# Kernel tuning notes

Hardware: AMD Instinct MI355X
Metric: run time of the kernel (lower is better)

Reference implementation:

```python
import jax, jax.numpy as jnp
import numpy as np

EPS = 1e-12  # F.normalize default eps (norm clamped to at least eps)


def setup_inputs() -> dict:
    key = jax.random.key(0)
    k1, k2, k3, k4 = jax.random.split(key, 4)
    B, Cin, Cout, H, W = 8, 128, 32, 256, 256
    x = jax.random.normal(k1, (B, Cin, H, W), dtype=jnp.float32)
    qk = jax.random.normal(k2, (B, 2 * Cout, H, W), dtype=jnp.float32)
    # 1x1 conv params (PyTorch Conv2d default init scale ~ 1/sqrt(fan_in))
    w_v = jax.random.normal(k3, (Cout, Cin), dtype=jnp.float32) / np.sqrt(Cin)
    b_v = jax.random.normal(k4, (Cout,), dtype=jnp.float32) / np.sqrt(Cin)
    temperature = jnp.ones((1, 1, 1), dtype=jnp.float32)
    return {"x": x, "qk": qk, "w_v": w_v, "b_v": b_v, "temperature": temperature}


def reference(x, qk, w_v, b_v, temperature):
    B, Cin, H, W = x.shape
    Co = w_v.shape[0]
    N = H * W
    # 1x1 conv == channel GEMM
    v = jnp.einsum('bchw,oc->bohw', x, w_v) + b_v[None, :, None, None]
    # split qk: k = first Co channels, q = last Co channels; head=1
    q = qk[:, Co:].reshape(B, 1, Co, N)
    k = qk[:, :Co].reshape(B, 1, Co, N)
    v = v.reshape(B, 1, Co, N)
    # L2-normalize over spatial dim (F.normalize: divide by max(norm, eps))
    q = q / jnp.maximum(jnp.linalg.norm(q, axis=-1, keepdims=True), EPS)
    k = k / jnp.maximum(jnp.linalg.norm(k, axis=-1, keepdims=True), EPS)
    # channel-wise (transposed) attention: [B,1,Co,Co]
    attn = jnp.einsum('bhcn,bhdn->bhcd', q, k) * temperature
    attn = jax.nn.softmax(attn, axis=-1)
    out = jnp.einsum('bhcd,bhdn->bhcn', attn, v)  # [B,1,Co,N]
    return out
```

## Files before the change

### kernel.cpp

```cpp
#include <hip/hip_runtime.h>
#include <math.h>

#define NB    8
#define CIN   128
#define CO    32
#define CH    64
#define NN    65536
#define CHUNKS 128
#define COLS_PB (NN/CHUNKS)
#define TILE  32
#define LSTR  72

__global__ __launch_bounds__(256) void gram_kernel(const float* __restrict__ qk,
                                                   float* __restrict__ part,
                                                   float* __restrict__ partsq) {
    __shared__ float lds[TILE * LSTR];
    __shared__ float red[4 * 1024 + 4 * 64];

    const int t = threadIdx.x;
    const int b = blockIdx.y;
    const int chunk = blockIdx.x;

    const int c = t >> 2;
    const int g = t & 3;

    const int w = t >> 6;
    const int lane = t & 63;
    const int l16 = lane & 15;
    const int colsub = lane >> 4;
    const int qi0 = 32 + (l16 >> 2) * 8;
    const int ki0 = (l16 & 3) * 8;

    const float* src = qk + (size_t)b * CH * NN + (size_t)chunk * COLS_PB + (size_t)c * NN;

    float acc[8][8];
#pragma unroll
    for (int i = 0; i < 8; ++i)
#pragma unroll
        for (int j = 0; j < 8; ++j) acc[i][j] = 0.f;
    float sqa[4] = {0.f, 0.f, 0.f, 0.f};

    for (int tile = 0; tile < COLS_PB / TILE; ++tile) {
        const float4* s4 = (const float4*)(src + tile * TILE);
        float4 v0 = s4[g * 2];
        float4 v1 = s4[g * 2 + 1];

        __syncthreads();
        float* dst = &lds[(g * 8) * LSTR + c];
        dst[0 * LSTR] = v0.x; dst[1 * LSTR] = v0.y; dst[2 * LSTR] = v0.z; dst[3 * LSTR] = v0.w;
        dst[4 * LSTR] = v1.x; dst[5 * LSTR] = v1.y; dst[6 * LSTR] = v1.z; dst[7 * LSTR] = v1.w;
        __syncthreads();

#pragma unroll
        for (int p = 0; p < 2; ++p) {
            const float* row = &lds[(w * 8 + p * 4 + colsub) * LSTR];
            float4 q0 = *(const float4*)(row + qi0);
            float4 q1 = *(const float4*)(row + qi0 + 4);
            float4 k0 = *(const float4*)(row + ki0);
            float4 k1 = *(const float4*)(row + ki0 + 4);
            float qv[8] = {q0.x, q0.y, q0.z, q0.w, q1.x, q1.y, q1.z, q1.w};
            float kv[8] = {k0.x, k0.y, k0.z, k0.w, k1.x, k1.y, k1.z, k1.w};
#pragma unroll
            for (int i = 0; i < 8; ++i)
#pragma unroll
                for (int j = 0; j < 8; ++j)
                    acc[i][j] = fmaf(qv[i], kv[j], acc[i][j]);
            float4 sv = *(const float4*)(row + l16 * 4);
            sqa[0] = fmaf(sv.x, sv.x, sqa[0]);
            sqa[1] = fmaf(sv.y, sv.y, sqa[1]);
            sqa[2] = fmaf(sv.z, sv.z, sqa[2]);
            sqa[3] = fmaf(sv.w, sv.w, sqa[3]);
        }
    }

#pragma unroll
    for (int i = 0; i < 8; ++i)
#pragma unroll
        for (int j = 0; j < 8; ++j) {
            acc[i][j] += __shfl_xor(acc[i][j], 16);
            acc[i][j] += __shfl_xor(acc[i][j], 32);
        }
#pragma unroll
    for (int s = 0; s < 4; ++s) {
        sqa[s] += __shfl_xor(sqa[s], 16);
        sqa[s] += __shfl_xor(sqa[s], 32);
    }

    if (colsub == 0) {
#pragma unroll
        for (int i = 0; i < 8; ++i)
#pragma unroll
            for (int j = 0; j < 8; ++j)
                red[w * 1024 + l16 * 64 + i * 8 + j] = acc[i][j];
#pragma unroll
        for (int s = 0; s < 4; ++s)
            red[4096 + w * 64 + l16 * 4 + s] = sqa[s];
    }
    __syncthreads();

    for (int idx = t; idx < 1024; idx += 256) {
        float s = red[idx] + red[1024 + idx] + red[2048 + idx] + red[3072 + idx];
        int lw = idx >> 6;
        int i = (idx >> 3) & 7;
        int j = idx & 7;
        int qrel = (lw >> 2) * 8 + i;
        int krel = (lw & 3) * 8 + j;
        part[((size_t)b * CHUNKS + chunk) * 1024 + qrel * 32 + krel] = s;
    }
    if (t < 64) {
        float s = red[4096 + t] + red[4096 + 64 + t] + red[4096 + 128 + t] + red[4096 + 192 + t];
        partsq[((size_t)b * CHUNKS + chunk) * 64 + t] = s;
    }
}

__global__ __launch_bounds__(128) void reduce_kernel(const float* __restrict__ part,
                                                     const float* __restrict__ partsq,
                                                     float* __restrict__ Sred) {
    const int b = blockIdx.y;
    const int v = blockIdx.x * 64 + (threadIdx.x >> 1);
    const int h = threadIdx.x & 1;
    float s = 0.f;
    if (v < 1024) {
        const float* p = part + (size_t)b * CHUNKS * 1024 + v;
        for (int ch = h * (CHUNKS / 2); ch < (h + 1) * (CHUNKS / 2); ++ch)
            s += p[(size_t)ch * 1024];
    } else {
        const float* p = partsq + (size_t)b * CHUNKS * 64 + (v - 1024);
        for (int ch = h * (CHUNKS / 2); ch < (h + 1) * (CHUNKS / 2); ++ch)
            s += p[(size_t)ch * 64];
    }
    s += __shfl_xor(s, 1);
    if (h == 0) Sred[b * 1088 + v] = s;
}

__global__ __launch_bounds__(256) void attn_kernel(const float* __restrict__ Sred,
                                                   const float* __restrict__ w_v,
                                                   const float* __restrict__ b_v,
                                                   const float* __restrict__ temp,
                                                   float* __restrict__ Weff,
                                                   float* __restrict__ beff) {
    __shared__ float sS[1024];
    __shared__ float snorm[64];
    __shared__ float sA[1024];
    const int t = threadIdx.x;
    const int b = blockIdx.x;

    for (int i = t; i < 1024; i += 256) sS[i] = Sred[b * 1088 + i];
    if (t < 64) snorm[t] = fmaxf(sqrtf(Sred[b * 1088 + 1024 + t]), 1e-12f);
    __syncthreads();

    if (t < 32) {
        const float T = temp[0];
        const float qn = snorm[32 + t];
        float m = -1e30f;
        for (int d = 0; d < 32; ++d)
            m = fmaxf(m, sS[t * 32 + d] / (qn * snorm[d]) * T);
        float sum = 0.f;
        for (int d = 0; d < 32; ++d)
            sum += expf(sS[t * 32 + d] / (qn * snorm[d]) * T - m);
        const float inv = 1.f / sum;
        for (int d = 0; d < 32; ++d)
            sA[t * 32 + d] = expf(sS[t * 32 + d] / (qn * snorm[d]) * T - m) * inv;
    }
    __syncthreads();

    for (int idx = t; idx < CO * CIN; idx += 256) {
        int cc = idx >> 7;
        int ci = idx & 127;
        float s = 0.f;
#pragma unroll
        for (int d = 0; d < 32; ++d) s += sA[cc * 32 + d] * w_v[d * CIN + ci];
        Weff[(size_t)b * CO * CIN + idx] = s;
    }
    if (t < 32) {
        float s = 0.f;
#pragma unroll
        for (int d = 0; d < 32; ++d) s += sA[t * 32 + d] * b_v[d];
        beff[b * CO + t] = s;
    }
}

__global__ __launch_bounds__(256) void out_kernel(const float* __restrict__ x,
                                                  const float* __restrict__ Weff,
                                                  const float* __restrict__ beff,
                                                  float* __restrict__ out) {
    const int b = blockIdx.y;
    const int n0 = blockIdx.x * 512 + threadIdx.x * 2;
    const float* xb = x + (size_t)b * CIN * NN + n0;
    const float* Wb = Weff + (size_t)b * CO * CIN;
    const float* bb = beff + b * CO;

    float a0[CO], a1[CO];
#pragma unroll
    for (int o = 0; o < CO; ++o) { a0[o] = bb[o]; a1[o] = bb[o]; }

#pragma unroll 4
    for (int ci = 0; ci < CIN; ++ci) {
        float2 xv = *(const float2*)(xb + (size_t)ci * NN);
#pragma unroll
        for (int o = 0; o < CO; ++o) {
            float wv = Wb[o * CIN + ci];
            a0[o] = fmaf(wv, xv.x, a0[o]);
            a1[o] = fmaf(wv, xv.y, a1[o]);
        }
    }

    float* ob = out + (size_t)b * CO * NN + n0;
#pragma unroll
    for (int o = 0; o < CO; ++o) {
        float2 r;
        r.x = a0[o];
        r.y = a1[o];
        *(float2*)(ob + (size_t)o * NN) = r;
    }
}

extern "C" void kernel_launch(void* const* d_in, const int* in_sizes, int n_in,
                              void* d_out, int out_size, void* d_ws, size_t ws_size,
                              hipStream_t stream) {
    const float* x    = (const float*)d_in[0];
    const float* qk   = (const float*)d_in[1];
    const float* w_v  = (const float*)d_in[2];
    const float* b_v  = (const float*)d_in[3];
    const float* temp = (const float*)d_in[4];
    float* out = (float*)d_out;

    float* part   = (float*)d_ws;
    float* partsq = part + (size_t)NB * CHUNKS * 1024;
    float* Sred   = partsq + (size_t)NB * CHUNKS * 64;
    float* Weff   = Sred + (size_t)NB * 1088;
    float* beff   = Weff + (size_t)NB * CO * CIN;

    gram_kernel<<<dim3(CHUNKS, NB), 256, 0, stream>>>(qk, part, partsq);
    reduce_kernel<<<dim3(17, NB), 128, 0, stream>>>(part, partsq, Sred);
    attn_kernel<<<dim3(NB), 256, 0, stream>>>(Sred, w_v, b_v, temp, Weff, beff);
    out_kernel<<<dim3(NN / 512, NB), 256, 0, stream>>>(x, Weff, beff, out);
}
```

Before: 133.2 us.

## Fuse partial reduction into attention kernel and retile output GEMM with LDS weights

```diff
diff --git a/kernel.cpp b/kernel.cpp
--- a/kernel.cpp
+++ b/kernel.cpp
@@ -113,40 +113,35 @@
     }
 }
 
-__global__ __launch_bounds__(128) void reduce_kernel(const float* __restrict__ part,
-                                                     const float* __restrict__ partsq,
-                                                     float* __restrict__ Sred) {
-    const int b = blockIdx.y;
-    const int v = blockIdx.x * 64 + (threadIdx.x >> 1);
-    const int h = threadIdx.x & 1;
-    float s = 0.f;
-    if (v < 1024) {
-        const float* p = part + (size_t)b * CHUNKS * 1024 + v;
-        for (int ch = h * (CHUNKS / 2); ch < (h + 1) * (CHUNKS / 2); ++ch)
-            s += p[(size_t)ch * 1024];
-    } else {
-        const float* p = partsq + (size_t)b * CHUNKS * 64 + (v - 1024);
-        for (int ch = h * (CHUNKS / 2); ch < (h + 1) * (CHUNKS / 2); ++ch)
-            s += p[(size_t)ch * 64];
-    }
-    s += __shfl_xor(s, 1);
-    if (h == 0) Sred[b * 1088 + v] = s;
-}
-
-__global__ __launch_bounds__(256) void attn_kernel(const float* __restrict__ Sred,
-                                                   const float* __restrict__ w_v,
-                                                   const float* __restrict__ b_v,
-                                                   const float* __restrict__ temp,
-                                                   float* __restrict__ Weff,
-                                                   float* __restrict__ beff) {
+__global__ __launch_bounds__(256) void finalize_kernel(const float* __restrict__ part,
+                                                       const float* __restrict__ partsq,
+                                                       const float* __restrict__ w_v,
+                                                       const float* __restrict__ b_v,
+                                                       const float* __restrict__ temp,
+                                                       float* __restrict__ Weff,
+                                                       float* __restrict__ beff) {
     __shared__ float sS[1024];
     __shared__ float snorm[64];
     __shared__ float sA[1024];
     const int t = threadIdx.x;
     const int b = blockIdx.x;
 
-    for (int i = t; i < 1024; i += 256) sS[i] = Sred[b * 1088 + i];
-    if (t < 64) snorm[t] = fmaxf(sqrtf(Sred[b * 1088 + 1024 + t]), 1e-12f);
+    for (int v = t; v < 1024; v += 256) {
+        const float* p = part + (size_t)b * CHUNKS * 1024 + v;
+        float s = 0.f;
+#pragma unroll 16
+        for (int ch = 0; ch < CHUNKS; ++ch)
+            s += p[(size_t)ch * 1024];
+        sS[v] = s;
+    }
+    if (t < 64) {
+        const float* p = partsq + (size_t)b * CHUNKS * 64 + t;
+        float s = 0.f;
+#pragma unroll 16
+        for (int ch = 0; ch < CHUNKS; ++ch)
+            s += p[(size_t)ch * 64];
+        snorm[t] = fmaxf(sqrtf(s), 1e-12f);
+    }
     __syncthreads();
 
     if (t < 32) {
@@ -184,35 +179,58 @@
                                                   const float* __restrict__ Weff,
                                                   const float* __restrict__ beff,
                                                   float* __restrict__ out) {
+    __shared__ float4 lw[CO * 32];
     const int b = blockIdx.y;
-    const int n0 = blockIdx.x * 512 + threadIdx.x * 2;
+    const int t = threadIdx.x;
+
+    {
+        const float4* Wb4 = (const float4*)(Weff + (size_t)b * CO * CIN);
+        for (int i = t; i < CO * 32; i += 256) lw[i] = Wb4[i];
+    }
+    __syncthreads();
+
+    const int n0 = blockIdx.x * 1024 + t * 4;
     const float* xb = x + (size_t)b * CIN * NN + n0;
-    const float* Wb = Weff + (size_t)b * CO * CIN;
     const float* bb = beff + b * CO;
 
-    float a0[CO], a1[CO];
-#pragma unroll
-    for (int o = 0; o < CO; ++o) { a0[o] = bb[o]; a1[o] = bb[o]; }
-
-#pragma unroll 4
-    for (int ci = 0; ci < CIN; ++ci) {
-        float2 xv = *(const float2*)(xb + (size_t)ci * NN);
+    float4 acc[CO];
+#pragma unroll
+    for (int o = 0; o < CO; ++o) {
+        float bv = bb[o];
+        acc[o] = make_float4(bv, bv, bv, bv);
+    }
+
+    for (int ci4 = 0; ci4 < 32; ++ci4) {
+        float4 xv0 = *(const float4*)(xb + (size_t)(ci4 * 4 + 0) * NN);
+        float4 xv1 = *(const float4*)(xb + (size_t)(ci4 * 4 + 1) * NN);
+        float4 xv2 = *(const float4*)(xb + (size_t)(ci4 * 4 + 2) * NN);
+        float4 xv3 = *(const float4*)(xb + (size_t)(ci4 * 4 + 3) * NN);
 #pragma unroll
         for (int o = 0; o < CO; ++o) {
-            float wv = Wb[o * CIN + ci];
-            a0[o] = fmaf(wv, xv.x, a0[o]);
-            a1[o] = fmaf(wv, xv.y, a1[o]);
+            float4 w = lw[o * 32 + ci4];
+            acc[o].x = fmaf(w.x, xv0.x, acc[o].x);
+            acc[o].y = fmaf(w.x, xv0.y, acc[o].y);
+            acc[o].z = fmaf(w.x, xv0.z, acc[o].z);
+            acc[o].w = fmaf(w.x, xv0.w, acc[o].w);
+            acc[o].x = fmaf(w.y, xv1.x, acc[o].x);
+            acc[o].y = fmaf(w.y, xv1.y, acc[o].y);
+            acc[o].z = fmaf(w.y, xv1.z, acc[o].z);
+            acc[o].w = fmaf(w.y, xv1.w, acc[o].w);
+            acc[o].x = fmaf(w.z, xv2.x, acc[o].x);
+            acc[o].y = fmaf(w.z, xv2.y, acc[o].y);
+            acc[o].z = fmaf(w.z, xv2.z, acc[o].z);
+            acc[o].w = fmaf(w.z, xv2.w, acc[o].w);
+            acc[o].x = fmaf(w.w, xv3.x, acc[o].x);
+            acc[o].y = fmaf(w.w, xv3.y, acc[o].y);
+            acc[o].z = fmaf(w.w, xv3.z, acc[o].z);
+            acc[o].w = fmaf(w.w, xv3.w, acc[o].w);
         }
     }
 
     float* ob = out + (size_t)b * CO * NN + n0;
 #pragma unroll
-    for (int o = 0; o < CO; ++o) {
-        float2 r;
-        r.x = a0[o];
-        r.y = a1[o];
-        *(float2*)(ob + (size_t)o * NN) = r;
-    }
+    for (int o = 0; o < CO; ++o)
+        *(float4*)(ob + (size_t)o * NN) = acc[o];
 }
 
 extern "C" void kernel_launch(void* const* d_in, const int* in_sizes, int n_in,
@@ -227,12 +245,10 @@
 
     float* part   = (float*)d_ws;
     float* partsq = part + (size_t)NB * CHUNKS * 1024;
-    float* Sred   = partsq + (size_t)NB * CHUNKS * 64;
-    float* Weff   = Sred + (size_t)NB * 1088;
+    float* Weff   = partsq + (size_t)NB * CHUNKS * 64;
     float* beff   = Weff + (size_t)NB * CO * CIN;
 
     gram_kernel<<<dim3(CHUNKS, NB), 256, 0, stream>>>(qk, part, partsq);
-    reduce_kernel<<<dim3(17, NB), 128, 0, stream>>>(part, partsq, Sred);
-    attn_kernel<<<dim3(NB), 256, 0, stream>>>(Sred, w_v, b_v, temp, Weff, beff);
-    out_kernel<<<dim3(NN / 512, NB), 256, 0, stream>>>(x, Weff, beff, out);
-}
+    finalize_kernel<<<dim3(NB), 256, 0, stream>>>(part, partsq, w_v, b_v, temp, Weff, beff);
+    out_kernel<<<dim3(NN / 1024, NB), 256, 0, stream>>>(x, Weff, beff, out);
+}
```

Result: slower. 161.2 us (+21.0%).

## Compute Gram matrix with split-bf16 MFMA per wave instead of LDS FMA tiles

Applied to the files above, without the earlier changes.

```diff
diff --git a/kernel.cpp b/kernel.cpp
--- a/kernel.cpp
+++ b/kernel.cpp
@@ -1,4 +1,5 @@
 #include <hip/hip_runtime.h>
+#include <hip/hip_bf16.h>
 #include <math.h>
 
 #define NB    8
@@ -7,109 +8,82 @@
 #define CH    64
 #define NN    65536
 #define CHUNKS 128
-#define COLS_PB (NN/CHUNKS)
-#define TILE  32
-#define LSTR  72
+#define GXB   32
+#define SPW   (NN/CHUNKS)
+#define SLABS (SPW/16)
+
+typedef __attribute__((ext_vector_type(8))) short bf16x8;
+typedef __attribute__((ext_vector_type(16))) float f32x16;
+
+__device__ __forceinline__ short f2bf(float f) {
+    union { __hip_bfloat16 h; short s; } u;
+    u.h = __float2bfloat16(f);
+    return u.s;
+}
+__device__ __forceinline__ float bf2f(short s) {
+    union { __hip_bfloat16 h; short s; } u;
+    u.s = s;
+    return __bfloat162float(u.h);
+}
 
 __global__ __launch_bounds__(256) void gram_kernel(const float* __restrict__ qk,
                                                    float* __restrict__ part,
                                                    float* __restrict__ partsq) {
-    __shared__ float lds[TILE * LSTR];
-    __shared__ float red[4 * 1024 + 4 * 64];
-
-    const int t = threadIdx.x;
     const int b = blockIdx.y;
-    const int chunk = blockIdx.x;
-
-    const int c = t >> 2;
-    const int g = t & 3;
-
-    const int w = t >> 6;
-    const int lane = t & 63;
-    const int l16 = lane & 15;
-    const int colsub = lane >> 4;
-    const int qi0 = 32 + (l16 >> 2) * 8;
-    const int ki0 = (l16 & 3) * 8;
-
-    const float* src = qk + (size_t)b * CH * NN + (size_t)chunk * COLS_PB + (size_t)c * NN;
-
-    float acc[8][8];
-#pragma unroll
-    for (int i = 0; i < 8; ++i)
-#pragma unroll
-        for (int j = 0; j < 8; ++j) acc[i][j] = 0.f;
-    float sqa[4] = {0.f, 0.f, 0.f, 0.f};
-
-    for (int tile = 0; tile < COLS_PB / TILE; ++tile) {
-        const float4* s4 = (const float4*)(src + tile * TILE);
-        float4 v0 = s4[g * 2];
-        float4 v1 = s4[g * 2 + 1];
-
-        __syncthreads();
-        float* dst = &lds[(g * 8) * LSTR + c];
-        dst[0 * LSTR] = v0.x; dst[1 * LSTR] = v0.y; dst[2 * LSTR] = v0.z; dst[3 * LSTR] = v0.w;
-        dst[4 * LSTR] = v1.x; dst[5 * LSTR] = v1.y; dst[6 * LSTR] = v1.z; dst[7 * LSTR] = v1.w;
-        __syncthreads();
-
-#pragma unroll
-        for (int p = 0; p < 2; ++p) {
-            const float* row = &lds[(w * 8 + p * 4 + colsub) * LSTR];
-            float4 q0 = *(const float4*)(row + qi0);
-            float4 q1 = *(const float4*)(row + qi0 + 4);
-            float4 k0 = *(const float4*)(row + ki0);
-            float4 k1 = *(const float4*)(row + ki0 + 4);
-            float qv[8] = {q0.x, q0.y, q0.z, q0.w, q1.x, q1.y, q1.z, q1.w};
-            float kv[8] = {k0.x, k0.y, k0.z, k0.w, k1.x, k1.y, k1.z, k1.w};
-#pragma unroll
-            for (int i = 0; i < 8; ++i)
-#pragma unroll
-                for (int j = 0; j < 8; ++j)
-                    acc[i][j] = fmaf(qv[i], kv[j], acc[i][j]);
-            float4 sv = *(const float4*)(row + l16 * 4);
-            sqa[0] = fmaf(sv.x, sv.x, sqa[0]);
-            sqa[1] = fmaf(sv.y, sv.y, sqa[1]);
-            sqa[2] = fmaf(sv.z, sv.z, sqa[2]);
-            sqa[3] = fmaf(sv.w, sv.w, sqa[3]);
+    const int w = threadIdx.x >> 6;
+    const int l = threadIdx.x & 63;
+    const int chunk = blockIdx.x * 4 + w;
+    const int c = l & 31;
+    const int half = l >> 5;
+
+    const float* qrow = qk + (size_t)b * CH * NN + (size_t)(CO + c) * NN
+                        + (size_t)chunk * SPW + half * 8;
+    const float* krow = qk + (size_t)b * CH * NN + (size_t)c * NN
+                        + (size_t)chunk * SPW + half * 8;
+
+    f32x16 acc = {};
+    float sqq = 0.f, sqk = 0.f;
+
+#pragma unroll 4
+    for (int s = 0; s < SLABS; ++s) {
+        float4 q0 = *(const float4*)(qrow + s * 16);
+        float4 q1 = *(const float4*)(qrow + s * 16 + 4);
+        float4 k0 = *(const float4*)(krow + s * 16);
+        float4 k1 = *(const float4*)(krow + s * 16 + 4);
+
+        float qf[8] = {q0.x, q0.y, q0.z, q0.w, q1.x, q1.y, q1.z, q1.w};
+        float kf[8] = {k0.x, k0.y, k0.z, k0.w, k1.x, k1.y, k1.z, k1.w};
+
+        bf16x8 ah, al, bh, bl;
+#pragma unroll
+        for (int j = 0; j < 8; ++j) {
+            short hq = f2bf(qf[j]);
+            ah[j] = hq;
+            al[j] = f2bf(qf[j] - bf2f(hq));
+            short hk = f2bf(kf[j]);
+            bh[j] = hk;
+            bl[j] = f2bf(kf[j] - bf2f(hk));
+            sqq = fmaf(qf[j], qf[j], sqq);
+            sqk = fmaf(kf[j], kf[j], sqk);
         }
-    }
-
-#pragma unroll
-    for (int i = 0; i < 8; ++i)
-#pragma unroll
-        for (int j = 0; j < 8; ++j) {
-            acc[i][j] += __shfl_xor(acc[i][j], 16);
-            acc[i][j] += __shfl_xor(acc[i][j], 32);
-        }
-#pragma unroll
-    for (int s = 0; s < 4; ++s) {
-        sqa[s] += __shfl_xor(sqa[s], 16);
-        sqa[s] += __shfl_xor(sqa[s], 32);
-    }
-
-    if (colsub == 0) {
-#pragma unroll
-        for (int i = 0; i < 8; ++i)
-#pragma unroll
-            for (int j = 0; j < 8; ++j)
-                red[w * 1024 + l16 * 64 + i * 8 + j] = acc[i][j];
-#pragma unroll
-        for (int s = 0; s < 4; ++s)
-            red[4096 + w * 64 + l16 * 4 + s] = sqa[s];
-    }
-    __syncthreads();
-
-    for (int idx = t; idx < 1024; idx += 256) {
-        float s = red[idx] + red[1024 + idx] + red[2048 + idx] + red[3072 + idx];
-        int lw = idx >> 6;
-        int i = (idx >> 3) & 7;
-        int j = idx & 7;
-        int qrel = (lw >> 2) * 8 + i;
-        int krel = (lw & 3) * 8 + j;
-        part[((size_t)b * CHUNKS + chunk) * 1024 + qrel * 32 + krel] = s;
-    }
-    if (t < 64) {
-        float s = red[4096 + t] + red[4096 + 64 + t] + red[4096 + 128 + t] + red[4096 + 192 + t];
-        partsq[((size_t)b * CHUNKS + chunk) * 64 + t] = s;
+        acc = __builtin_amdgcn_mfma_f32_32x32x16_bf16(ah, bh, acc, 0, 0, 0);
+        acc = __builtin_amdgcn_mfma_f32_32x32x16_bf16(ah, bl, acc, 0, 0, 0);
+        acc = __builtin_amdgcn_mfma_f32_32x32x16_bf16(al, bh, acc, 0, 0, 0);
+    }
+
+    sqq += __shfl_xor(sqq, 32);
+    sqk += __shfl_xor(sqk, 32);
+    if (half == 0) {
+        float* psq = partsq + ((size_t)b * CHUNKS + chunk) * 64;
+        psq[c] = sqk;
+        psq[CO + c] = sqq;
+    }
+
+    float* pp = part + ((size_t)b * CHUNKS + chunk) * 1024;
+#pragma unroll
+    for (int r = 0; r < 16; ++r) {
+        int row = (r & 3) + 8 * (r >> 2) + 4 * half;
+        pp[row * 32 + c] = acc[r];
     }
 }
 
@@ -231,7 +205,7 @@
     float* Weff   = Sred + (size_t)NB * 1088;
     float* beff   = Weff + (size_t)NB * CO * CIN;
 
-    gram_kernel<<<dim3(CHUNKS, NB), 256, 0, stream>>>(qk, part, partsq);
+    gram_kernel<<<dim3(GXB, NB), 256, 0, stream>>>(qk, part, partsq);
     reduce_kernel<<<dim3(17, NB), 128, 0, stream>>>(part, partsq, Sred);
     attn_kernel<<<dim3(NB), 256, 0, stream>>>(Sred, w_v, b_v, temp, Weff, beff);
     out_kernel<<<dim3(NN / 512, NB), 256, 0, stream>>>(x, Weff, beff, out);
```

Result: faster. 119.9 us (-10.0%).
